# Performance work log

Hardware: AMD Instinct MI355X
Metric: run time of the kernel (lower is better)

Reference implementation:

```python
import jax, jax.numpy as jnp
import numpy as np


def setup_inputs() -> dict:
    key = jax.random.key(0)
    ks = jax.random.split(key, 8)
    B, Cin, Cattr, Cout, H, W = 8, 256, 256, 256, 64, 64
    x = jax.random.normal(ks[0], (B, Cin, H, W), dtype=jnp.float32)
    attr = jax.random.normal(ks[1], (B, Cattr, H, W), dtype=jnp.float32)
    # 1x1 conv weights stored as [out, in] (kernel_size=1 squeezed)
    sq = 1.0 / np.sqrt(Cin)
    sa = 1.0 / np.sqrt(Cattr)
    Wq = jax.random.uniform(ks[2], (Cout, Cin), jnp.float32, -sq, sq)
    bq = jax.random.uniform(ks[3], (Cout,), jnp.float32, -sq, sq)
    Wk = jax.random.uniform(ks[4], (Cout, Cattr), jnp.float32, -sa, sa)
    bk = jax.random.uniform(ks[5], (Cout,), jnp.float32, -sa, sa)
    Wv = jax.random.uniform(ks[6], (Cout, Cattr), jnp.float32, -sa, sa)
    bv = jax.random.uniform(ks[7], (Cout,), jnp.float32, -sa, sa)
    return {"x": x, "attr": attr, "Wq": Wq, "bq": bq, "Wk": Wk, "bk": bk, "Wv": Wv, "bv": bv}


def reference(x, attr, Wq, bq, Wk, bk, Wv, bv):
    B, Cin, H, W = x.shape
    # 1x1 convs == per-pixel linear projections
    q = jnp.einsum('bchw,oc->bohw', x, Wq) + bq[None, :, None, None]      # [B,C,H,W]
    k = jnp.einsum('bchw,oc->bohw', attr, Wk) + bk[None, :, None, None]
    v = jnp.einsum('bchw,oc->bohw', attr, Wv) + bv[None, :, None, None]
    C = q.shape[1]
    qf = q.reshape(B, C, H * W)   # [B,C,N]
    kf = k.reshape(B, C, H * W)
    vf = v.reshape(B, C, H * W)
    # attn[b,i,j] = sum_c q[b,c,i] * k[b,c,j]  -> softmax over j
    attn = jax.nn.softmax(jnp.einsum('bci,bcj->bij', qf, kf), axis=-1)    # [B,N,N]
    out = jnp.einsum('bcj,bij->bci', vf, attn)                            # [B,C,N]
    return out.reshape(B, C, H, W) + x
```

## Files before the change

### kernel.cpp

```cpp
#include <hip/hip_runtime.h>

typedef _Float16 f16;
typedef _Float16 f16x8 __attribute__((ext_vector_type(8)));
typedef _Float16 f16x4 __attribute__((ext_vector_type(4)));
typedef float f32x4 __attribute__((ext_vector_type(4)));
typedef float f32x16 __attribute__((ext_vector_type(16)));

#define LOG2E 1.44269504088896340736f
#define SOFF  36.0f
#define CDIM 256
#define NPIX 4096

__device__ __forceinline__ void gl2lds16(const f16* g, const f16* l) {
    __builtin_amdgcn_global_load_lds((const __attribute__((address_space(1))) unsigned int*)g,
                                     (__attribute__((address_space(3))) unsigned int*)l, 16, 0, 0);
}

__global__ void convert_w_kernel(const float* __restrict__ Wq, const float* __restrict__ Wk,
                                 const float* __restrict__ Wv,
                                 f16* __restrict__ Wq_h, f16* __restrict__ Wk_h,
                                 f16* __restrict__ Wv_h) {
    int i = blockIdx.x * 256 + threadIdx.x;
    Wq_h[i] = (f16)(Wq[i] * LOG2E);
    Wk_h[i] = (f16)Wk[i];
    Wv_h[i] = (f16)Wv[i];
}

__global__ __launch_bounds__(256, 2)
void proj_kernel(const float* __restrict__ x, const float* __restrict__ attr,
                 const f16* __restrict__ Wq_h, const float* __restrict__ bq,
                 const f16* __restrict__ Wk_h, const float* __restrict__ bk,
                 const f16* __restrict__ Wv_h, const float* __restrict__ bv,
                 f16* __restrict__ qT, f16* __restrict__ kT, f16* __restrict__ vW) {
    __shared__ __align__(16) f16 Xs[64 * 256];
    __shared__ __align__(16) f16 As[64 * 256];

    const int b  = blockIdx.x & 7;
    const int i0 = (blockIdx.x >> 3) * 64;
    const int t  = threadIdx.x;
    const int w = t >> 6, lane = t & 63, l31 = lane & 31, hi = lane >> 5;
    const int xorv = l31 & 7;

    {
        const int i  = t & 63;
        const int cb = t >> 6;
        const float* xb = x    + (size_t)b * CDIM * NPIX + i0 + i;
        const float* ab = attr + (size_t)b * CDIM * NPIX + i0 + i;
#pragma unroll 2
        for (int rep = 0; rep < 8; ++rep) {
            int chunk = cb * 8 + rep;
            const float* xs = xb + (size_t)(chunk * 8) * NPIX;
            const float* as_ = ab + (size_t)(chunk * 8) * NPIX;
            f16x8 xv, av;
#pragma unroll
            for (int e = 0; e < 8; ++e) {
                xv[e] = (f16)xs[(size_t)e * NPIX];
                av[e] = (f16)as_[(size_t)e * NPIX];
            }
            int phys = chunk ^ (i & 7);
            *(f16x8*)(Xs + i * 256 + phys * 8) = xv;
            *(f16x8*)(As + i * 256 + phys * 8) = av;
        }
    }
    __syncthreads();

#pragma unroll 1
    for (int k = 0; k < 12; ++k) {
        const int tt = w + 4 * k;
        const int kind = tt >> 4;
        const int rr = tt & 15;
        const int ct = rr >> 1;
        const int half = rr & 1;

        const f16* Wm = (kind == 0) ? Wq_h : ((kind == 1) ? Wk_h : Wv_h);
        const f16* Bs = (kind == 0) ? Xs : As;
        const float* bias = (kind == 0) ? bq : ((kind == 1) ? bk : bv);
        const float bscale = (kind == 0) ? LOG2E : 1.0f;

        const f16* ap = Wm + (size_t)(ct * 32 + l31) * CDIM + hi * 8;
        const f16* bp = Bs + (half * 32 + l31) * 256;

        f32x16 acc;
#pragma unroll
        for (int r = 0; r < 16; ++r) acc[r] = 0.0f;
#pragma unroll
        for (int ks = 0; ks < 16; ++ks) {
            f16x8 afr = *(const f16x8*)(ap + ks * 16);
            f16x8 bfr = *(const f16x8*)(bp + (((2 * ks + hi) ^ xorv)) * 8);
            acc = __builtin_amdgcn_mfma_f32_32x32x16_f16(afr, bfr, acc, 0, 0, 0);
        }

        const int nidx = i0 + half * 32 + l31;
        if (kind < 2) {
            f16* dst = ((kind == 0) ? qT : kT)
                       + ((size_t)b * NPIX + nidx) * CDIM + ct * 32 + 4 * hi;
#pragma unroll
            for (int g = 0; g < 4; ++g) {
                f32x4 bb = *(const f32x4*)(bias + ct * 32 + 4 * hi + 8 * g);
                f16x4 pk;
#pragma unroll
                for (int e = 0; e < 4; ++e) pk[e] = (f16)(acc[4 * g + e] + bb[e] * bscale);
                *(f16x4*)(dst + 8 * g) = pk;
            }
        } else {
            f16* dst = vW + (size_t)b * CDIM * NPIX + nidx;
#pragma unroll
            for (int g = 0; g < 4; ++g) {
                f32x4 bb = *(const f32x4*)(bias + ct * 32 + 4 * hi + 8 * g);
#pragma unroll
                for (int e = 0; e < 4; ++e) {
                    int c = ct * 32 + 4 * hi + 8 * g + e;
                    dst[(size_t)c * NPIX] = (f16)(acc[4 * g + e] + bb[e]);
                }
            }
        }
    }
}

__global__ __launch_bounds__(512, 2)
void attn_kernel(const f16* __restrict__ qT, const f16* __restrict__ kT,
                 const f16* __restrict__ vW, const float* __restrict__ x,
                 float* __restrict__ out) {
    extern __shared__ unsigned char smem[];

    const int b    = blockIdx.x & 7;
    const int i0   = (blockIdx.x >> 3) * 128;
    const int t    = threadIdx.x;
    const int w    = t >> 6;
    const int lane = t & 63;
    const int l31  = lane & 31;
    const int hi   = lane >> 5;
    const int iw   = (w & 3) * 32;
    const int jh   = (w >> 2) * 32;
    const int jh8  = (w >> 2) * 4;
    const int ig   = i0 + iw + l31;
    const int xorv = l31 & 7;

    f16x8 qf[16];
    {
        const f16* qp = qT + ((size_t)b * NPIX + ig) * CDIM + hi * 8;
#pragma unroll
        for (int ks = 0; ks < 16; ++ks) qf[ks] = *(const f16x8*)(qp + ks * 16);
    }

    int kp4o[4];
    {
        int kboff = (jh + l31) * 256 + (hi ^ (xorv & 1)) * 8;
        const int xv2 = xorv >> 1;
#pragma unroll
        for (int r = 0; r < 4; ++r) kp4o[r] = kboff + (r ^ xv2) * 16;
    }
    int vp2o[2];
    {
        int vboff = 16384 + l31 * 64;
#pragma unroll
        for (int kj = 0; kj < 2; ++kj) vp2o[kj] = vboff + (((jh8 + 2 * kj + hi) ^ xorv)) * 8;
    }

    f32x16 acc[8];
#pragma unroll
    for (int ct = 0; ct < 8; ++ct)
#pragma unroll
        for (int r = 0; r < 16; ++r) acc[ct][r] = 0.0f;
    float lrun = 0.0f;

    const f16* kb = kT + (size_t)b * NPIX * CDIM;
    const f16* vb = vW + (size_t)b * CDIM * NPIX;
    f16* lds0 = (f16*)smem;
    const int wub = (t & ~63) * 8;

    {
#pragma unroll
        for (int rep = 0; rep < 4; ++rep) {
            int slot = t + rep * 512;
            int krow = slot >> 5, kpc = slot & 31;
            gl2lds16(kb + (size_t)krow * CDIM + ((kpc ^ (krow & 7)) * 8),
                     lds0 + wub + rep * 4096);
            int vrow = slot >> 3, vpc = slot & 7;
            gl2lds16(vb + (size_t)vrow * NPIX + ((vpc ^ (vrow & 7)) * 8),
                     lds0 + 16384 + wub + rep * 4096);
        }
    }

    union Q4 { f16x4 h; unsigned int u[2]; };
    union B8 { f16x8 h; unsigned int u[4]; };

#pragma unroll 1
    for (int jt = 0; jt < 64; ++jt) {
        const int p = jt & 1;
        __syncthreads();

        if (jt < 63) {
            const int j0n = (jt + 1) * 64;
            f16* dstb = lds0 + (p ^ 1) * 32768;
#pragma unroll
            for (int rep = 0; rep < 4; ++rep) {
                int slot = t + rep * 512;
                int krow = slot >> 5, kpc = slot & 31;
                gl2lds16(kb + (size_t)(j0n + krow) * CDIM + ((kpc ^ (krow & 7)) * 8),
                         dstb + wub + rep * 4096);
                int vrow = slot >> 3, vpc = slot & 7;
                gl2lds16(vb + (size_t)vrow * NPIX + j0n + ((vpc ^ (vrow & 7)) * 8),
                         dstb + 16384 + wub + rep * 4096);
            }
        }

        const f16* L = lds0 + p * 32768;

        f32x16 s;
#pragma unroll
        for (int r = 0; r < 16; ++r) s[r] = -SOFF;
#pragma unroll
        for (int ks = 0; ks < 16; ++ks)
            s = __builtin_amdgcn_mfma_f32_32x32x16_f16(
                *(const f16x8*)(L + kp4o[ks & 3] + (ks >> 2) * 64), qf[ks], s, 0, 0, 0);

        Q4 ownq[4];
        float rtot = 0.0f;
#pragma unroll
        for (int g = 0; g < 4; ++g) {
            float p0 = __builtin_amdgcn_exp2f(s[4 * g + 0]);
            float p1 = __builtin_amdgcn_exp2f(s[4 * g + 1]);
            float p2 = __builtin_amdgcn_exp2f(s[4 * g + 2]);
            float p3 = __builtin_amdgcn_exp2f(s[4 * g + 3]);
            rtot += (p0 + p1) + (p2 + p3);
            ownq[g].h[0] = (f16)p0; ownq[g].h[1] = (f16)p1;
            ownq[g].h[2] = (f16)p2; ownq[g].h[3] = (f16)p3;
        }
        lrun += rtot;

        f16x8 pb[2];
#pragma unroll
        for (int kj = 0; kj < 2; ++kj) {
            int sidx = 2 * kj + 1 - hi;
            int oidx = 2 * kj + hi;
            unsigned int s0 = ownq[sidx].u[0], s1 = ownq[sidx].u[1];
            unsigned int r0 = (unsigned int)__shfl_xor((int)s0, 32);
            unsigned int r1 = (unsigned int)__shfl_xor((int)s1, 32);
            B8 bb;
            bb.u[0] = hi ? r0 : ownq[oidx].u[0];
            bb.u[1] = hi ? r1 : ownq[oidx].u[1];
            bb.u[2] = hi ? ownq[oidx].u[0] : r0;
            bb.u[3] = hi ? ownq[oidx].u[1] : r1;
            pb[kj] = bb.h;
        }

#pragma unroll
        for (int ct = 0; ct < 8; ++ct) {
            acc[ct] = __builtin_amdgcn_mfma_f32_32x32x16_f16(
                *(const f16x8*)(L + vp2o[0] + ct * 2048), pb[0], acc[ct], 0, 0, 0);
            acc[ct] = __builtin_amdgcn_mfma_f32_32x32x16_f16(
                *(const f16x8*)(L + vp2o[1] + ct * 2048), pb[1], acc[ct], 0, 0, 0);
        }
    }

    float lsum = lrun + __shfl_xor(lrun, 32);
    __syncthreads();
    float* Obuf = (float*)smem;
    float* Ls   = (float*)(smem + 131072);
    if (w >= 4) {
        float* ob = Obuf + (w - 4) * 8192;
#pragma unroll
        for (int ct = 0; ct < 8; ++ct)
#pragma unroll
            for (int r = 0; r < 16; ++r) {
                int c = ct * 32 + (r & 3) + 8 * (r >> 2) + 4 * hi;
                ob[c * 32 + l31] = acc[ct][r];
            }
        if (hi == 0) Ls[(w - 4) * 32 + l31] = lsum;
    }
    __syncthreads();
    if (w < 4) {
        const float ltot = lsum + Ls[w * 32 + l31];
        const float invl = 1.0f / ltot;
        const float* po = Obuf + w * 8192;
        const float* xb = x + (size_t)b * CDIM * NPIX + i0 + iw;
        float* og = out + (size_t)b * CDIM * NPIX + i0 + iw;
#pragma unroll
        for (int ct = 0; ct < 8; ++ct)
#pragma unroll
            for (int r = 0; r < 16; ++r) {
                int c = ct * 32 + (r & 3) + 8 * (r >> 2) + 4 * hi;
                size_t off = (size_t)c * NPIX + l31;
                og[off] = (acc[ct][r] + po[c * 32 + l31]) * invl + xb[off];
            }
    }
}

extern "C" void kernel_launch(void* const* d_in, const int* in_sizes, int n_in,
                              void* d_out, int out_size, void* d_ws, size_t ws_size,
                              hipStream_t stream) {
    const float* x    = (const float*)d_in[0];
    const float* attr = (const float*)d_in[1];
    const float* Wq   = (const float*)d_in[2];
    const float* bq   = (const float*)d_in[3];
    const float* Wk   = (const float*)d_in[4];
    const float* bk   = (const float*)d_in[5];
    const float* Wv   = (const float*)d_in[6];
    const float* bv   = (const float*)d_in[7];
    float* out = (float*)d_out;

    char* ws = (char*)d_ws;
    const size_t qkv_bytes = (size_t)8 * NPIX * CDIM * sizeof(f16);
    f16* qT   = (f16*)ws;
    f16* kT   = (f16*)(ws + qkv_bytes);
    f16* vW   = (f16*)(ws + 2 * qkv_bytes);
    f16* Wq_h = (f16*)(ws + 3 * qkv_bytes);
    f16* Wk_h = Wq_h + 65536;
    f16* Wv_h = Wk_h + 65536;

    (void)hipFuncSetAttribute((const void*)attn_kernel,
                              hipFuncAttributeMaxDynamicSharedMemorySize, 131584);

    convert_w_kernel<<<256, 256, 0, stream>>>(Wq, Wk, Wv, Wq_h, Wk_h, Wv_h);
    proj_kernel<<<512, 256, 0, stream>>>(x, attr, Wq_h, bq, Wk_h, bk, Wv_h, bv, qT, kT, vW);
    attn_kernel<<<256, 512, 131584, stream>>>(qT, kT, vW, x, out);
}
```

Measured before the change: 320.9 us.

## Pre-swizzle V and weights into MFMA fragment order, load V directly to registers

The projection kernel now writes V in a fragment-major layout so each lane of the attention kernel can load its MFMA A-operand for V with contiguous 16-byte global loads. This removes V from the LDS double buffer, halving its footprint and the associated sync traffic. V loads are software-prefetched one channel tile ahead. Weights are likewise pre-packed into per-lane fragment order for coalesced loads in the projection kernel. The trade is that V now streams from global/L2 on every tile with no LDS reuse across waves, which risks exposed memory latency.

```diff
diff --git a/kernel.cpp b/kernel.cpp
--- a/kernel.cpp
+++ b/kernel.cpp
@@ -18,20 +18,32 @@
 
 __global__ void convert_w_kernel(const float* __restrict__ Wq, const float* __restrict__ Wk,
                                  const float* __restrict__ Wv,
-                                 f16* __restrict__ Wq_h, f16* __restrict__ Wk_h,
-                                 f16* __restrict__ Wv_h) {
-    int i = blockIdx.x * 256 + threadIdx.x;
-    Wq_h[i] = (f16)(Wq[i] * LOG2E);
-    Wk_h[i] = (f16)Wk[i];
-    Wv_h[i] = (f16)Wv[i];
+                                 f16* __restrict__ WqF, f16* __restrict__ WkF,
+                                 f16* __restrict__ WvF) {
+    int t = blockIdx.x * 256 + threadIdx.x;
+    int m = t >> 13;
+    int g = t & 8191;
+    int lane = g & 63;
+    int ksct = g >> 6;
+    int ks = ksct & 15, ct = ksct >> 4;
+    int o = ct * 32 + (lane & 31);
+    int cin0 = ks * 16 + (lane >> 5) * 8;
+    const float* W = (m == 0) ? Wq : ((m == 1) ? Wk : Wv);
+    f16* WF = (m == 0) ? WqF : ((m == 1) ? WkF : WvF);
+    const float scale = (m == 0) ? LOG2E : 1.0f;
+    const float* src = W + (size_t)o * CDIM + cin0;
+    f16x8 v;
+#pragma unroll
+    for (int e = 0; e < 8; ++e) v[e] = (f16)(src[e] * scale);
+    *(f16x8*)(WF + (size_t)g * 8) = v;
 }
 
 __global__ __launch_bounds__(256, 2)
 void proj_kernel(const float* __restrict__ x, const float* __restrict__ attr,
-                 const f16* __restrict__ Wq_h, const float* __restrict__ bq,
-                 const f16* __restrict__ Wk_h, const float* __restrict__ bk,
-                 const f16* __restrict__ Wv_h, const float* __restrict__ bv,
-                 f16* __restrict__ qT, f16* __restrict__ kT, f16* __restrict__ vW) {
+                 const f16* __restrict__ WqF, const float* __restrict__ bq,
+                 const f16* __restrict__ WkF, const float* __restrict__ bk,
+                 const f16* __restrict__ WvF, const float* __restrict__ bv,
+                 f16* __restrict__ qT, f16* __restrict__ kT, f16* __restrict__ vF) {
     __shared__ __align__(16) f16 Xs[64 * 256];
     __shared__ __align__(16) f16 As[64 * 256];
 
@@ -72,12 +84,12 @@
         const int ct = rr >> 1;
         const int half = rr & 1;
 
-        const f16* Wm = (kind == 0) ? Wq_h : ((kind == 1) ? Wk_h : Wv_h);
+        const f16* WF = (kind == 0) ? WqF : ((kind == 1) ? WkF : WvF);
         const f16* Bs = (kind == 0) ? Xs : As;
         const float* bias = (kind == 0) ? bq : ((kind == 1) ? bk : bv);
         const float bscale = (kind == 0) ? LOG2E : 1.0f;
 
-        const f16* ap = Wm + (size_t)(ct * 32 + l31) * CDIM + hi * 8;
+        const f16* ap = WF + (size_t)(ct * 16) * 512 + (size_t)lane * 8;
         const f16* bp = Bs + (half * 32 + l31) * 256;
 
         f32x16 acc;
@@ -85,7 +97,7 @@
         for (int r = 0; r < 16; ++r) acc[r] = 0.0f;
 #pragma unroll
         for (int ks = 0; ks < 16; ++ks) {
-            f16x8 afr = *(const f16x8*)(ap + ks * 16);
+            f16x8 afr = *(const f16x8*)(ap + ks * 512);
             f16x8 bfr = *(const f16x8*)(bp + (((2 * ks + hi) ^ xorv)) * 8);
             acc = __builtin_amdgcn_mfma_f32_32x32x16_f16(afr, bfr, acc, 0, 0, 0);
         }
@@ -103,14 +115,15 @@
                 *(f16x4*)(dst + 8 * g) = pk;
             }
         } else {
-            f16* dst = vW + (size_t)b * CDIM * NPIX + nidx;
+            const int jpart = ((nidx >> 4) << 9) + (((nidx >> 3) & 1) << 8) + (nidx & 7);
+            f16* vb2 = vF + (size_t)b * CDIM * NPIX + (size_t)ct * 131072 + jpart;
 #pragma unroll
             for (int g = 0; g < 4; ++g) {
                 f32x4 bb = *(const f32x4*)(bias + ct * 32 + 4 * hi + 8 * g);
 #pragma unroll
                 for (int e = 0; e < 4; ++e) {
-                    int c = ct * 32 + 4 * hi + 8 * g + e;
-                    dst[(size_t)c * NPIX] = (f16)(acc[4 * g + e] + bb[e]);
+                    int c31 = 4 * hi + 8 * g + e;
+                    vb2[c31 * 8] = (f16)(acc[4 * g + e] + bb[e]);
                 }
             }
         }
@@ -119,7 +132,7 @@
 
 __global__ __launch_bounds__(512, 2)
 void attn_kernel(const f16* __restrict__ qT, const f16* __restrict__ kT,
-                 const f16* __restrict__ vW, const float* __restrict__ x,
+                 const f16* __restrict__ vF, const float* __restrict__ x,
                  float* __restrict__ out) {
     extern __shared__ unsigned char smem[];
 
@@ -132,7 +145,7 @@
     const int hi   = lane >> 5;
     const int iw   = (w & 3) * 32;
     const int jh   = (w >> 2) * 32;
-    const int jh8  = (w >> 2) * 4;
+    const int jh16 = (w >> 2) * 2;
     const int ig   = i0 + iw + l31;
     const int xorv = l31 & 7;
 
@@ -150,12 +163,6 @@
 #pragma unroll
         for (int r = 0; r < 4; ++r) kp4o[r] = kboff + (r ^ xv2) * 16;
     }
-    int vp2o[2];
-    {
-        int vboff = 16384 + l31 * 64;
-#pragma unroll
-        for (int kj = 0; kj < 2; ++kj) vp2o[kj] = vboff + (((jh8 + 2 * kj + hi) ^ xorv)) * 8;
-    }
 
     f32x16 acc[8];
 #pragma unroll
@@ -164,8 +171,8 @@
         for (int r = 0; r < 16; ++r) acc[ct][r] = 0.0f;
     float lrun = 0.0f;
 
-    const f16* kb = kT + (size_t)b * NPIX * CDIM;
-    const f16* vb = vW + (size_t)b * CDIM * NPIX;
+    const f16* kb  = kT + (size_t)b * NPIX * CDIM;
+    const f16* vbJ = vF + (size_t)b * CDIM * NPIX;
     f16* lds0 = (f16*)smem;
     const int wub = (t & ~63) * 8;
 
@@ -176,9 +183,6 @@
             int krow = slot >> 5, kpc = slot & 31;
             gl2lds16(kb + (size_t)krow * CDIM + ((kpc ^ (krow & 7)) * 8),
                      lds0 + wub + rep * 4096);
-            int vrow = slot >> 3, vpc = slot & 7;
-            gl2lds16(vb + (size_t)vrow * NPIX + ((vpc ^ (vrow & 7)) * 8),
-                     lds0 + 16384 + wub + rep * 4096);
         }
     }
 
@@ -190,22 +194,25 @@
         const int p = jt & 1;
         __syncthreads();
 
+        const f16* vjt = vbJ + (size_t)jt * 2048 + (lane << 3) + (jh16 << 9);
+        f16x8 vx0 = *(const f16x8*)(vjt);
+        f16x8 vx1 = *(const f16x8*)(vjt + 512);
+        f16x8 vy0 = *(const f16x8*)(vjt + 131072);
+        f16x8 vy1 = *(const f16x8*)(vjt + 131072 + 512);
+
         if (jt < 63) {
             const int j0n = (jt + 1) * 64;
-            f16* dstb = lds0 + (p ^ 1) * 32768;
+            f16* dstb = lds0 + (p ^ 1) * 16384;
 #pragma unroll
             for (int rep = 0; rep < 4; ++rep) {
                 int slot = t + rep * 512;
                 int krow = slot >> 5, kpc = slot & 31;
                 gl2lds16(kb + (size_t)(j0n + krow) * CDIM + ((kpc ^ (krow & 7)) * 8),
                          dstb + wub + rep * 4096);
-                int vrow = slot >> 3, vpc = slot & 7;
-                gl2lds16(vb + (size_t)vrow * NPIX + j0n + ((vpc ^ (vrow & 7)) * 8),
-                         dstb + 16384 + wub + rep * 4096);
-            }
-        }
-
-        const f16* L = lds0 + p * 32768;
+            }
+        }
+
+        const f16* L = lds0 + p * 16384;
 
         f32x16 s;
 #pragma unroll
@@ -247,10 +254,16 @@
 
 #pragma unroll
         for (int ct = 0; ct < 8; ++ct) {
-            acc[ct] = __builtin_amdgcn_mfma_f32_32x32x16_f16(
-                *(const f16x8*)(L + vp2o[0] + ct * 2048), pb[0], acc[ct], 0, 0, 0);
-            acc[ct] = __builtin_amdgcn_mfma_f32_32x32x16_f16(
-                *(const f16x8*)(L + vp2o[1] + ct * 2048), pb[1], acc[ct], 0, 0, 0);
+            f16x8 c0 = (ct & 1) ? vy0 : vx0;
+            f16x8 c1 = (ct & 1) ? vy1 : vx1;
+            if (ct < 6) {
+                const f16* np = vjt + (size_t)(ct + 2) * 131072;
+                f16x8 n0 = *(const f16x8*)(np);
+                f16x8 n1 = *(const f16x8*)(np + 512);
+                if (ct & 1) { vy0 = n0; vy1 = n1; } else { vx0 = n0; vx1 = n1; }
+            }
+            acc[ct] = __builtin_amdgcn_mfma_f32_32x32x16_f16(c0, pb[0], acc[ct], 0, 0, 0);
+            acc[ct] = __builtin_amdgcn_mfma_f32_32x32x16_f16(c1, pb[1], acc[ct], 0, 0, 0);
         }
     }
 
@@ -304,15 +317,15 @@
     const size_t qkv_bytes = (size_t)8 * NPIX * CDIM * sizeof(f16);
     f16* qT   = (f16*)ws;
     f16* kT   = (f16*)(ws + qkv_bytes);
-    f16* vW   = (f16*)(ws + 2 * qkv_bytes);
-    f16* Wq_h = (f16*)(ws + 3 * qkv_bytes);
-    f16* Wk_h = Wq_h + 65536;
-    f16* Wv_h = Wk_h + 65536;
+    f16* vF   = (f16*)(ws + 2 * qkv_bytes);
+    f16* WqF  = (f16*)(ws + 3 * qkv_bytes);
+    f16* WkF  = WqF + 65536;
+    f16* WvF  = WkF + 65536;
 
     (void)hipFuncSetAttribute((const void*)attn_kernel,
                               hipFuncAttributeMaxDynamicSharedMemorySize, 131584);
 
-    convert_w_kernel<<<256, 256, 0, stream>>>(Wq, Wk, Wv, Wq_h, Wk_h, Wv_h);
-    proj_kernel<<<512, 256, 0, stream>>>(x, attr, Wq_h, bq, Wk_h, bk, Wv_h, bv, qT, kT, vW);
-    attn_kernel<<<256, 512, 131584, stream>>>(qT, kT, vW, x, out);
-}
+    convert_w_kernel<<<96, 256, 0, stream>>>(Wq, Wk, Wv, WqF, WkF, WvF);
+    proj_kernel<<<512, 256, 0, stream>>>(x, attr, WqF, bq, WkF, bk, WvF, bv, qT, kT, vF);
+    attn_kernel<<<256, 512, 131584, stream>>>(qT, kT, vF, x, out);
+}
```

Measured after the change: 326.8 us. About the same (+1.8%).
